# Kernel tuning notes

Hardware: AMD Instinct MI355X
Metric: run time of the kernel (lower is better)

## Reference

```python
import jax, jax.numpy as jnp
import numpy as np

RANK = 64
VOCAB = 32768
BATCH = 2048
SEQLEN = 256


def setup_inputs() -> dict:
    key = jax.random.key(0)
    k1, k2, k3, k4 = jax.random.split(key, 4)
    # scale so born-squared core matrices have ~unit spectral growth per step
    s = RANK ** -0.5
    return {
        "y": jax.random.randint(k1, (BATCH, SEQLEN), 0, VOCAB, dtype=jnp.int32),
        "alpha": jax.random.normal(k2, (1, RANK), jnp.float32),
        "beta": jax.random.normal(k3, (1, RANK), jnp.float32),
        "core": jax.random.normal(k4, (1, RANK, VOCAB, RANK), jnp.float32) * s,
    }


def reference(y, alpha, beta, core):
    """MPSDist.get_unnorm_prob with born parametrization.

    p_tilde(y)[b] = alpha^2 @ prod_t core^2[:, y[b,t], :] @ beta^2
    Sequential left-to-right uMPS contraction (same recurrence the sampler
    runs at every decode step), expressed as a lax.scan carrying the
    (batch, rank) left boundary vector.
    """
    a = (alpha ** 2)[0]                     # (R,)
    b = (beta ** 2)[0]                      # (R,)
    c = (core ** 2)[0]                      # (R, V, R)
    batch = y.shape[0]
    l0 = jnp.broadcast_to(a, (batch, a.shape[0]))  # (B, R)
    ys = y.T                                # (T, B) -> scan over time

    def step(l, y_t):
        A = c[:, y_t, :]                    # (R, B, R) selected core slices
        l = jnp.einsum("br,rbs->bs", l, A)  # carry left boundary
        return l, None

    lT, _ = jax.lax.scan(step, l0, ys)
    return lT @ b                           # (B,) unnormalized probs
```

## Files before the change

### kernel.cpp

```cpp
#include <hip/hip_runtime.h>

#define RANK   64
#define VOCAB  32768
#define BATCH  2048
#define SEQLEN 256

typedef __attribute__((ext_vector_type(4))) unsigned int uint4v;

#define WS_DATA_BYTES ((size_t)VOCAB * 5120)
#define WS_SC_BYTES   ((size_t)VOCAB * 256)

__global__ __launch_bounds__(64) void squash10_kernel(const float* __restrict__ core,
                                                      unsigned int* __restrict__ wsd,
                                                      float* __restrict__ wssc) {
    __shared__ float tsq[64 * 65];
    __shared__ float tinv[64];

    const int v = blockIdx.x;
    const int s = threadIdx.x;

    float sq[64];
#pragma unroll
    for (int r = 0; r < 64; ++r) {
        float c = __builtin_nontemporal_load(&core[((size_t)r * VOCAB + v) * RANK + s]);
        sq[r] = c * c;
    }
#pragma unroll
    for (int r = 0; r < 64; ++r) tsq[r * 65 + s] = sq[r];
    __syncthreads();

    float mx = 0.f;
#pragma unroll
    for (int q = 0; q < 64; ++q) mx = fmaxf(mx, tsq[s * 65 + q]);
    float scale = mx * (1.0f / 1023.0f);
    float inv   = (mx > 0.f) ? (1023.0f / mx) : 0.f;
    wssc[(size_t)v * 64 + s] = scale;
    tinv[s] = inv;
    __syncthreads();

    unsigned int D[20];
#pragma unroll
    for (int gi = 0; gi < 4; ++gi) {
        unsigned int e[16];
#pragma unroll
        for (int q = 0; q < 16; ++q) {
            float qq = sq[16 * gi + q] * tinv[16 * gi + q];
            unsigned int u = (unsigned int)(qq + 0.5f);
            e[q] = (u > 1023u) ? 1023u : u;
        }
        D[5 * gi + 0] = e[0] | (e[1] << 10) | (e[2] << 20) | (e[3] << 30);
        D[5 * gi + 1] = (e[3] >> 2) | (e[4] << 8) | (e[5] << 18) | (e[6] << 28);
        D[5 * gi + 2] = (e[6] >> 4) | (e[7] << 6) | (e[8] << 16) | (e[9] << 26);
        D[5 * gi + 3] = (e[9] >> 6) | (e[10] << 4) | (e[11] << 14) | (e[12] << 24);
        D[5 * gi + 4] = (e[12] >> 8) | (e[13] << 2) | (e[14] << 12) | (e[15] << 22);
    }
    uint4v* dst = (uint4v*)wsd;
#pragma unroll
    for (int c = 0; c < 5; ++c) {
        uint4v w;
        w[0] = D[4 * c + 0]; w[1] = D[4 * c + 1];
        w[2] = D[4 * c + 2]; w[3] = D[4 * c + 3];
        dst[((size_t)v * 5 + c) * 64 + s] = w;
    }
}

__device__ __forceinline__ void gload16(const void* g, void* l) {
    __builtin_amdgcn_global_load_lds(
        (const __attribute__((address_space(1))) void*)g,
        (__attribute__((address_space(3))) void*)l, 16, 0, 0);
}
__device__ __forceinline__ void gload4(const void* g, void* l) {
    __builtin_amdgcn_global_load_lds(
        (const __attribute__((address_space(1))) void*)g,
        (__attribute__((address_space(3))) void*)l, 4, 0, 0);
}

__global__ __launch_bounds__(64) void mps_u10_lds_kernel(const int* __restrict__ y,
                                                         const float* __restrict__ alpha,
                                                         const float* __restrict__ beta,
                                                         const unsigned int* __restrict__ wsd,
                                                         const float* __restrict__ wssc,
                                                         float* __restrict__ out) {
    __shared__ uint4v sdat[3][5][64];
    __shared__ float  ssc[3][64];

    const int b    = blockIdx.x;
    const int lane = threadIdx.x;
    const int* yrow = y + (size_t)b * SEQLEN;

    int yr0 = yrow[0 * 64 + lane];
    int yr1 = yrow[1 * 64 + lane];
    int yr2 = yrow[2 * 64 + lane];
    int yr3 = yrow[3 * 64 + lane];

    float a  = alpha[lane];
    float bb = beta[lane];
    float l  = a * a;
    float b2 = bb * bb;

    asm volatile("" :: "v"(yr1), "v"(yr2), "v"(yr3), "v"(b2), "v"(l));

    const uint4v* wsd4 = (const uint4v*)wsd;

    auto stage = [&](int kk, int slot) {
        int c_  = kk >> 6;
        int yy  = (c_ == 0) ? yr0 : (c_ == 1) ? yr1 : (c_ == 2) ? yr2 : yr3;
        int tok = __builtin_amdgcn_readlane(yy, kk & 63);
        const uint4v* gp = wsd4 + (size_t)tok * 320 + lane;
#pragma unroll
        for (int c = 0; c < 5; ++c) gload16(gp + c * 64, &sdat[slot][c][0]);
        gload4(wssc + (size_t)tok * 64 + lane, &ssc[slot][0]);
    };

    auto consume = [&](int slot) {
        float ls = l * ssc[slot][lane];
        unsigned int D[20];
#pragma unroll
        for (int c = 0; c < 5; ++c) {
            uint4v d = sdat[slot][c][lane];
            D[4 * c + 0] = d[0]; D[4 * c + 1] = d[1];
            D[4 * c + 2] = d[2]; D[4 * c + 3] = d[3];
        }
        float acc0 = 0.f, acc1 = 0.f, acc2 = 0.f, acc3 = 0.f;
#pragma unroll
        for (int gi = 0; gi < 4; ++gi) {
            unsigned int d0 = D[5 * gi + 0], d1 = D[5 * gi + 1],
                         d2 = D[5 * gi + 2], d3 = D[5 * gi + 3],
                         d4 = D[5 * gi + 4];
            unsigned int ee[16];
            ee[0]  = d0 & 1023u;
            ee[1]  = (d0 >> 10) & 1023u;
            ee[2]  = (d0 >> 20) & 1023u;
            ee[3]  = ((d0 >> 30) | (d1 << 2)) & 1023u;
            ee[4]  = (d1 >> 8) & 1023u;
            ee[5]  = (d1 >> 18) & 1023u;
            ee[6]  = ((d1 >> 28) | (d2 << 4)) & 1023u;
            ee[7]  = (d2 >> 6) & 1023u;
            ee[8]  = (d2 >> 16) & 1023u;
            ee[9]  = ((d2 >> 26) | (d3 << 6)) & 1023u;
            ee[10] = (d3 >> 4) & 1023u;
            ee[11] = (d3 >> 14) & 1023u;
            ee[12] = ((d3 >> 24) | (d4 << 8)) & 1023u;
            ee[13] = (d4 >> 2) & 1023u;
            ee[14] = (d4 >> 12) & 1023u;
            ee[15] = d4 >> 22;
#pragma unroll
            for (int q = 0; q < 16; ++q) {
                const int r = 16 * gi + q;
                float lr = __uint_as_float(
                    __builtin_amdgcn_readlane(__float_as_uint(ls), r));
                float mv = (float)ee[q];
                if ((q & 3) == 0)      acc0 = fmaf(lr, mv, acc0);
                else if ((q & 3) == 1) acc1 = fmaf(lr, mv, acc1);
                else if ((q & 3) == 2) acc2 = fmaf(lr, mv, acc2);
                else                   acc3 = fmaf(lr, mv, acc3);
            }
        }
        l = (acc0 + acc1) + (acc2 + acc3);
    };

    stage(0, 0);
    stage(1, 1);

#define STEP(S, SLOT, STSLOT)                                              \
    do {                                                                   \
        int kk = (S) + 2; kk = (kk > SEQLEN - 1) ? (SEQLEN - 1) : kk;      \
        stage(kk, (STSLOT));                                               \
        asm volatile("s_waitcnt vmcnt(12)" ::: "memory");                  \
        __builtin_amdgcn_sched_barrier(0);                                 \
        consume((SLOT));                                                   \
        asm volatile("s_waitcnt lgkmcnt(0)" ::: "memory");                 \
        __builtin_amdgcn_sched_barrier(0);                                 \
    } while (0)

#pragma unroll 1
    for (int t3 = 0; t3 < 85; ++t3) {
        int s0 = 3 * t3;
        STEP(s0 + 0, 0, 2);
        STEP(s0 + 1, 1, 0);
        STEP(s0 + 2, 2, 1);
    }
    asm volatile("s_waitcnt vmcnt(6)" ::: "memory");
    __builtin_amdgcn_sched_barrier(0);
    consume(0);
#undef STEP

    float v = l * b2;
#pragma unroll
    for (int off = 32; off > 0; off >>= 1) v += __shfl_xor(v, off, 64);
    if (lane == 0) out[b] = v;
}

__global__ __launch_bounds__(256) void mps_f32_kernel(const int* __restrict__ y,
                                                      const float* __restrict__ alpha,
                                                      const float* __restrict__ beta,
                                                      const float* __restrict__ core,
                                                      float* __restrict__ out) {
    int b    = (blockIdx.x * 256 + threadIdx.x) >> 6;
    int lane = threadIdx.x & 63;
    const int* yrow = y + (size_t)b * SEQLEN;

    float a = alpha[lane];
    float l = a * a;

#pragma unroll 1
    for (int t = 0; t < SEQLEN; ++t) {
        int tok = __builtin_amdgcn_readfirstlane(yrow[t]);
        const float* p = core + (size_t)tok * RANK + lane;
        float acc[4] = {0.f, 0.f, 0.f, 0.f};
#pragma unroll
        for (int r = 0; r < 64; ++r) {
            float m  = p[(size_t)r * (VOCAB * RANK)];
            float lr = __uint_as_float(
                __builtin_amdgcn_readlane(__float_as_uint(l), r));
            acc[r & 3] = fmaf(lr, m * m, acc[r & 3]);
        }
        l = (acc[0] + acc[1]) + (acc[2] + acc[3]);
    }

    float bb = beta[lane];
    float v  = l * bb * bb;
#pragma unroll
    for (int off = 32; off > 0; off >>= 1) v += __shfl_xor(v, off, 64);
    if (lane == 0) out[b] = v;
}

extern "C" void kernel_launch(void* const* d_in, const int* in_sizes, int n_in,
                              void* d_out, int out_size, void* d_ws, size_t ws_size,
                              hipStream_t stream) {
    const int*   y     = (const int*)d_in[0];
    const float* alpha = (const float*)d_in[1];
    const float* beta  = (const float*)d_in[2];
    const float* core  = (const float*)d_in[3];
    float*       out   = (float*)d_out;

    const size_t need = WS_DATA_BYTES + WS_SC_BYTES;

    if (ws_size >= need) {
        unsigned int* wsd  = (unsigned int*)d_ws;
        float*        wssc = (float*)((char*)d_ws + WS_DATA_BYTES);
        squash10_kernel<<<VOCAB, 64, 0, stream>>>(core, wsd, wssc);
        mps_u10_lds_kernel<<<BATCH, 64, 0, stream>>>(y, alpha, beta, wsd, wssc, out);
    } else {
        mps_f32_kernel<<<(BATCH * 64) / 256, 256, 0, stream>>>(
            y, alpha, beta, core, out);
    }
}
```

Measured before the change: 568.6 us.

## Replace global-to-LDS async loads with register-staged loads and explicit LDS writes

The per-step core slice and scale are now loaded from global memory into registers, then written to a rotating LDS slot after the current step's consume. This replaces the direct global_load_lds DMA path and the hand-tuned vmcnt/lgkmcnt waits. The intent is to let the compiler schedule ordinary loads and avoid LDS-DMA overheads. The cost is that the LDS write forces a wait on the load issued one step earlier, shortening the prefetch distance and raising register use.

```diff
diff --git a/kernel.cpp b/kernel.cpp
--- a/kernel.cpp
+++ b/kernel.cpp
@@ -64,18 +64,7 @@
     }
 }
 
-__device__ __forceinline__ void gload16(const void* g, void* l) {
-    __builtin_amdgcn_global_load_lds(
-        (const __attribute__((address_space(1))) void*)g,
-        (__attribute__((address_space(3))) void*)l, 16, 0, 0);
-}
-__device__ __forceinline__ void gload4(const void* g, void* l) {
-    __builtin_amdgcn_global_load_lds(
-        (const __attribute__((address_space(1))) void*)g,
-        (__attribute__((address_space(3))) void*)l, 4, 0, 0);
-}
-
-__global__ __launch_bounds__(64) void mps_u10_lds_kernel(const int* __restrict__ y,
+__global__ __launch_bounds__(64) void mps_u10_reg_kernel(const int* __restrict__ y,
                                                          const float* __restrict__ alpha,
                                                          const float* __restrict__ beta,
                                                          const unsigned int* __restrict__ wsd,
@@ -98,18 +87,31 @@
     float l  = a * a;
     float b2 = bb * bb;
 
-    asm volatile("" :: "v"(yr1), "v"(yr2), "v"(yr3), "v"(b2), "v"(l));
-
     const uint4v* wsd4 = (const uint4v*)wsd;
 
-    auto stage = [&](int kk, int slot) {
+    uint4v R0, R1, R2, R3, R4;
+    float  Rs;
+
+    auto loadregs = [&](int kk) {
         int c_  = kk >> 6;
         int yy  = (c_ == 0) ? yr0 : (c_ == 1) ? yr1 : (c_ == 2) ? yr2 : yr3;
         int tok = __builtin_amdgcn_readlane(yy, kk & 63);
         const uint4v* gp = wsd4 + (size_t)tok * 320 + lane;
-#pragma unroll
-        for (int c = 0; c < 5; ++c) gload16(gp + c * 64, &sdat[slot][c][0]);
-        gload4(wssc + (size_t)tok * 64 + lane, &ssc[slot][0]);
+        R0 = gp[0 * 64];
+        R1 = gp[1 * 64];
+        R2 = gp[2 * 64];
+        R3 = gp[3 * 64];
+        R4 = gp[4 * 64];
+        Rs = wssc[(size_t)tok * 64 + lane];
+    };
+
+    auto writeslot = [&](int slot) {
+        sdat[slot][0][lane] = R0;
+        sdat[slot][1][lane] = R1;
+        sdat[slot][2][lane] = R2;
+        sdat[slot][3][lane] = R3;
+        sdat[slot][4][lane] = R4;
+        ssc[slot][lane]     = Rs;
     };
 
     auto consume = [&](int slot) {
@@ -159,17 +161,19 @@
         l = (acc0 + acc1) + (acc2 + acc3);
     };
 
-    stage(0, 0);
-    stage(1, 1);
-
-#define STEP(S, SLOT, STSLOT)                                              \
+    loadregs(0); writeslot(0);
+    loadregs(1); writeslot(1);
+    loadregs(2);
+    __builtin_amdgcn_sched_barrier(0);
+
+#define STEP(S, CSLOT, WSLOT)                                              \
     do {                                                                   \
-        int kk = (S) + 2; kk = (kk > SEQLEN - 1) ? (SEQLEN - 1) : kk;      \
-        stage(kk, (STSLOT));                                               \
-        asm volatile("s_waitcnt vmcnt(12)" ::: "memory");                  \
+        consume((CSLOT));                                                  \
         __builtin_amdgcn_sched_barrier(0);                                 \
-        consume((SLOT));                                                   \
-        asm volatile("s_waitcnt lgkmcnt(0)" ::: "memory");                 \
+        writeslot((WSLOT));                      \
+        __builtin_amdgcn_sched_barrier(0);                                 \
+        int kk = (S) + 3; kk = (kk > SEQLEN - 1) ? (SEQLEN - 1) : kk;      \
+        loadregs(kk);                                                      \
         __builtin_amdgcn_sched_barrier(0);                                 \
     } while (0)
 
@@ -180,8 +184,6 @@
         STEP(s0 + 1, 1, 0);
         STEP(s0 + 2, 2, 1);
     }
-    asm volatile("s_waitcnt vmcnt(6)" ::: "memory");
-    __builtin_amdgcn_sched_barrier(0);
     consume(0);
 #undef STEP
 
@@ -240,7 +242,7 @@
         unsigned int* wsd  = (unsigned int*)d_ws;
         float*        wssc = (float*)((char*)d_ws + WS_DATA_BYTES);
         squash10_kernel<<<VOCAB, 64, 0, stream>>>(core, wsd, wssc);
-        mps_u10_lds_kernel<<<BATCH, 64, 0, stream>>>(y, alpha, beta, wsd, wssc, out);
+        mps_u10_reg_kernel<<<BATCH, 64, 0, stream>>>(y, alpha, beta, wsd, wssc, out);
     } else {
         mps_f32_kernel<<<(BATCH * 64) / 256, 256, 0, stream>>>(
             y, alpha, beta, core, out);
```

New measurement: 537.5 us (median of 3 runs). 5.5% less time.
